# Kernel tuning notes

Hardware: AMD Instinct MI355X
Metric: run time of the kernel (lower is better)

Reference implementation:

```python
import jax, jax.numpy as jnp
import numpy as np

NEG = 10000.0

def setup_inputs() -> dict:
    key = jax.random.key(0)
    ks = jax.random.split(key, 5)
    B, S, D = 2, 2048, 1024
    std = 1.0 / np.sqrt(D)
    return {
        "x": jax.random.normal(ks[0], (B, S, D), dtype=jnp.float32),
        "Wq": jax.random.normal(ks[1], (D, D), dtype=jnp.float32) * std,
        "bq": jnp.zeros((D,), jnp.float32),
        "Wk": jax.random.normal(ks[2], (D, D), dtype=jnp.float32) * std,
        "bk": jnp.zeros((D,), jnp.float32),
        "Wv": jax.random.normal(ks[3], (D, D), dtype=jnp.float32) * std,
        "bv": jnp.zeros((D,), jnp.float32),
        "Wo": jax.random.normal(ks[4], (D, D), dtype=jnp.float32) * std,
        "bo": jnp.zeros((D,), jnp.float32),
    }

def reference(x, Wq, bq, Wk, bk, Wv, bv, Wo, bo):
    # Linear projections + relu activation (as in the keras layer; note: no head split
    # is performed in this implementation, head_num is only a divisibility check).
    q = jax.nn.relu(x @ Wq + bq)  # [B,S,D]
    k = jax.nn.relu(x @ Wk + bk)
    v = jax.nn.relu(x @ Wv + bv)
    D = q.shape[-1]
    e = jnp.einsum('bqd,bkd->bqk', q, k) / jnp.sqrt(jnp.float32(D))  # [B,S,S]
    # history_only causal mask: penalize key positions j > query position i
    S = e.shape[-1]
    causal = (jnp.arange(S)[None, :] > jnp.arange(S)[:, None]).astype(e.dtype)
    e = e - NEG * causal[None, :, :]
    # stable softmax exactly as in the source (max-subtract, exp, normalize)
    e = jnp.exp(e - jnp.max(e, axis=-1, keepdims=True))
    attn = e / jnp.sum(e, axis=-1, keepdims=True)
    y = jnp.einsum('bqk,bkd->bqd', attn, v)
    return jax.nn.relu(y @ Wo + bo)
```

## Files before the change

kernel.cpp:

```cpp
#include <hip/hip_runtime.h>
#include <math.h>


typedef _Float16 f16x8 __attribute__((ext_vector_type(8)));
typedef float f32x4 __attribute__((ext_vector_type(4)));

#define BK 32

__device__ __forceinline__ void gload_lds16(const void* g, void* l) {
  __builtin_amdgcn_global_load_lds(
      (const __attribute__((address_space(1))) void*)g,
      (__attribute__((address_space(3))) void*)l, 16, 0, 0);
}

template<bool RELU, bool HAS_BIAS, int CAUSAL, int TMp, int TNp, bool MULTI, typename OT>
__global__ __launch_bounds__(256) void gemm_f16(
    const _Float16* __restrict__ A, const _Float16* __restrict__ BT,
    const float* __restrict__ bias0, const float* __restrict__ bias1,
    const float* __restrict__ bias2,
    OT* __restrict__ C0, OT* __restrict__ C1, OT* __restrict__ C2,
    int M, int Nout, int K, float scale,
    long long sA, long long sB, long long sC)
{
  int m0, n0;
  if (CAUSAL == 1) {
    int bx = blockIdx.x;
    int i = (int)((sqrtf(4.f * bx + 1.f) - 1.f) * 0.5f);
    while ((i + 1) * (i + 2) <= bx) ++i;
    while (i * (i + 1) > bx) --i;
    int j = bx - i * (i + 1);
    m0 = i * TMp;
    n0 = j * TNp;
  } else {
    m0 = blockIdx.y * TMp;
    n0 = blockIdx.x * TNp;
  }
  A  += (long long)blockIdx.z * sA;
  BT += (long long)blockIdx.z * sB;
  const int kend = (CAUSAL == 2) ? ((m0 + TMp < K) ? m0 + TMp : K) : K;

  __shared__ _Float16 Ah[TMp * BK];
  __shared__ _Float16 Bh[TNp * BK];

  const int tid  = threadIdx.x;
  const int lane = tid & 63;
  const int wid  = tid >> 6;
  const int wm   = (wid >> 1) * (TMp / 2);
  const int wn   = (wid & 1) * (TNp / 2);
  const int l15  = lane & 15;
  const int quad = lane >> 4;
  constexpr int MT = TMp / 32;
  constexpr int NT = TNp / 32;

  f32x4 acc[MT][NT];
  #pragma unroll
  for (int i = 0; i < MT; ++i)
    #pragma unroll
    for (int j = 0; j < NT; ++j)
      acc[i][j] = (f32x4){0.f, 0.f, 0.f, 0.f};

  constexpr int AI = TMp / 64;
  constexpr int BI = TNp / 64;
  const int ar = wid * (TMp / 4);
  const int br = wid * (TNp / 4);
  const int rl = lane >> 2;
  const int kq = (lane & 3) * 8;

  for (int k0 = 0; k0 < kend; k0 += BK) {
    #pragma unroll
    for (int t = 0; t < AI; ++t)
      gload_lds16(A + (long long)(m0 + ar + t * 16 + rl) * K + k0 + kq,
                  Ah + (ar + t * 16) * BK);
    #pragma unroll
    for (int t = 0; t < BI; ++t)
      gload_lds16(BT + (long long)(n0 + br + t * 16 + rl) * K + k0 + kq,
                  Bh + (br + t * 16) * BK);
    __syncthreads();

    const f16x8* ap = (const f16x8*)(Ah + (wm + l15) * BK + quad * 8);
    const f16x8* bp = (const f16x8*)(Bh + (wn + l15) * BK + quad * 8);
    f16x8 af[MT], bf[NT];
    #pragma unroll
    for (int t = 0; t < MT; ++t) af[t] = ap[t * 64];
    #pragma unroll
    for (int t = 0; t < NT; ++t) bf[t] = bp[t * 64];
    #pragma unroll
    for (int mt = 0; mt < MT; ++mt)
      #pragma unroll
      for (int nt = 0; nt < NT; ++nt)
        acc[mt][nt] = __builtin_amdgcn_mfma_f32_16x16x32_f16(
            af[mt], bf[nt], acc[mt][nt], 0, 0, 0);
    __syncthreads();
  }

  const int mat = MULTI ? (n0 / Nout) : 0;
  const float* bias = HAS_BIAS ? (mat == 0 ? bias0 : (mat == 1 ? bias1 : bias2)) : nullptr;
  OT* C = (mat == 0 ? C0 : (mat == 1 ? C1 : C2)) + (long long)blockIdx.z * sC;
  const int c0 = MULTI ? (n0 - mat * Nout) : n0;

  float bvals[NT];
  if (HAS_BIAS) {
    #pragma unroll
    for (int nt = 0; nt < NT; ++nt)
      bvals[nt] = bias[c0 + wn + nt * 16 + l15];
  }
  #pragma unroll
  for (int mt = 0; mt < MT; ++mt) {
    #pragma unroll
    for (int nt = 0; nt < NT; ++nt) {
      const int col = c0 + wn + nt * 16 + l15;
      #pragma unroll
      for (int r = 0; r < 4; ++r) {
        const int row = m0 + wm + mt * 16 + quad * 4 + r;
        float v = acc[mt][nt][r] * scale;
        if (HAS_BIAS) v += bvals[nt];
        if (RELU) v = fmaxf(v, 0.f);
        C[(long long)row * Nout + col] = (OT)v;
      }
    }
  }
}

__global__ __launch_bounds__(256) void cvt_f32_f16(
    const float* __restrict__ in, _Float16* __restrict__ out)
{
  const long long i = ((long long)blockIdx.x * 256 + threadIdx.x) * 8;
  float4 a = *(const float4*)(in + i);
  float4 b = *(const float4*)(in + i + 4);
  f16x8 o = {(_Float16)a.x, (_Float16)a.y, (_Float16)a.z, (_Float16)a.w,
             (_Float16)b.x, (_Float16)b.y, (_Float16)b.z, (_Float16)b.w};
  *(f16x8*)(out + i) = o;
}

__global__ __launch_bounds__(256) void cvtT_all(
    const float* __restrict__ W0, const float* __restrict__ W1,
    const float* __restrict__ W2, const float* __restrict__ W3,
    _Float16* __restrict__ WT, int K, int N)
{
  __shared__ _Float16 t[64][72];
  const int z = blockIdx.z;
  const float* W = (z == 0) ? W0 : (z == 1) ? W1 : (z == 2) ? W2 : W3;
  _Float16* dst = WT + (long long)z * K * N;
  const int k0 = blockIdx.x * 64, n0 = blockIdx.y * 64;
  const int tid = threadIdx.x;
  #pragma unroll
  for (int it = 0; it < 4; ++it) {
    int idx = tid + it * 256;
    int r = idx >> 4, c4 = (idx & 15) << 2;
    float4 w = *(const float4*)(W + (long long)(k0 + r) * N + n0 + c4);
    t[r][c4 + 0] = (_Float16)w.x; t[r][c4 + 1] = (_Float16)w.y;
    t[r][c4 + 2] = (_Float16)w.z; t[r][c4 + 3] = (_Float16)w.w;
  }
  __syncthreads();
  #pragma unroll
  for (int it = 0; it < 2; ++it) {
    int idx = tid + it * 256;
    int r = idx >> 3, c8 = (idx & 7) << 3;
    f16x8 o;
    #pragma unroll
    for (int j = 0; j < 8; ++j) o[j] = t[c8 + j][r];
    *(f16x8*)(dst + (long long)(n0 + r) * K + k0 + c8) = o;
  }
}

__global__ __launch_bounds__(256) void transp_f16(
    const _Float16* __restrict__ V, _Float16* __restrict__ VT, int S, int D)
{
  __shared__ _Float16 t[64][72];
  const _Float16* Vb = V + (long long)blockIdx.z * S * D;
  _Float16* VTb = VT + (long long)blockIdx.z * D * S;
  const int s0 = blockIdx.x * 64, d0 = blockIdx.y * 64;
  const int tid = threadIdx.x;
  #pragma unroll
  for (int it = 0; it < 2; ++it) {
    int idx = tid + it * 256;
    int r = idx >> 3, c8 = (idx & 7) << 3;
    f16x8 v = *(const f16x8*)(Vb + (long long)(s0 + r) * D + d0 + c8);
    *(f16x8*)&t[r][c8] = v;
  }
  __syncthreads();
  #pragma unroll
  for (int it = 0; it < 2; ++it) {
    int idx = tid + it * 256;
    int r = idx >> 3, c8 = (idx & 7) << 3;
    f16x8 o;
    #pragma unroll
    for (int j = 0; j < 8; ++j) o[j] = t[c8 + j][r];
    *(f16x8*)(VTb + (long long)(d0 + r) * S + s0 + c8) = o;
  }
}

__global__ __launch_bounds__(256) void softmax_causal_h(
    _Float16* __restrict__ E, int S)
{
  const int i = blockIdx.x;
  _Float16* row = E + ((long long)blockIdx.y * S + i) * S;
  const int tid = threadIdx.x;
  const int n = i + 1;
  const int j0 = tid * 8;

  f16x8 hv = *(const f16x8*)(row + j0);
  float vals[8];
  float m = -3.0e38f;
  #pragma unroll
  for (int t = 0; t < 8; ++t) {
    float v = (j0 + t < n) ? (float)hv[t] : -3.0e38f;
    vals[t] = v;
    m = fmaxf(m, v);
  }
  #pragma unroll
  for (int o = 32; o > 0; o >>= 1) m = fmaxf(m, __shfl_down(m, o, 64));

  __shared__ float rmax[4];
  __shared__ float rsum[4];
  const int wave = tid >> 6;
  if ((tid & 63) == 0) rmax[wave] = m;
  __syncthreads();
  m = fmaxf(fmaxf(rmax[0], rmax[1]), fmaxf(rmax[2], rmax[3]));

  float s = 0.f;
  #pragma unroll
  for (int t = 0; t < 8; ++t) {
    float e = (j0 + t < n) ? expf(vals[t] - m) : 0.f;
    vals[t] = e;
    s += e;
  }
  #pragma unroll
  for (int o = 32; o > 0; o >>= 1) s += __shfl_down(s, o, 64);
  if ((tid & 63) == 0) rsum[wave] = s;
  __syncthreads();
  s = rsum[0] + rsum[1] + rsum[2] + rsum[3];

  const float inv = 1.0f / s;
  f16x8 ov;
  #pragma unroll
  for (int t = 0; t < 8; ++t) ov[t] = (_Float16)(vals[t] * inv);
  *(f16x8*)(row + j0) = ov;
}

extern "C" void kernel_launch(void* const* d_in, const int* in_sizes, int n_in,
                              void* d_out, int out_size, void* d_ws, size_t ws_size,
                              hipStream_t stream) {
  const float* x  = (const float*)d_in[0];
  const float* Wq = (const float*)d_in[1];
  const float* bq = (const float*)d_in[2];
  const float* Wk = (const float*)d_in[3];
  const float* bk = (const float*)d_in[4];
  const float* Wv = (const float*)d_in[5];
  const float* bv = (const float*)d_in[6];
  const float* Wo = (const float*)d_in[7];
  const float* bo = (const float*)d_in[8];
  float* out = (float*)d_out;

  const int Bn = 2, S = 2048, D = 1024;
  const int M = Bn * S;
  const size_t MD = (size_t)M * D;
  const size_t DD = (size_t)D * D;
  const size_t SS = (size_t)Bn * S * S;

  _Float16* ws   = (_Float16*)d_ws;
  _Float16* xh   = ws;
  _Float16* Wcat = xh + MD;
  _Float16* Qh   = Wcat + 4 * DD;
  _Float16* Kh   = Qh + MD;
  _Float16* Vh   = Kh + MD;
  _Float16* VTh  = Vh + MD;
  _Float16* E    = VTh + MD;
  _Float16* Yh   = E + SS;

  dim3 blk(256);

  cvt_f32_f16<<<dim3((unsigned)(MD / 2048)), blk, 0, stream>>>(x, xh);
  cvtT_all<<<dim3(D / 64, D / 64, 4), blk, 0, stream>>>(Wq, Wk, Wv, Wo, Wcat, D, D);

  gemm_f16<true, true, 0, 128, 128, true, _Float16>
      <<<dim3(3 * D / 128, M / 128), blk, 0, stream>>>(
      xh, Wcat, bq, bk, bv, Qh, Kh, Vh, M, D, D, 1.0f, 0, 0, 0);

  transp_f16<<<dim3(S / 64, D / 64, Bn), blk, 0, stream>>>(Vh, VTh, S, D);

  gemm_f16<false, false, 1, 128, 64, false, _Float16>
      <<<dim3(272, 1, Bn), blk, 0, stream>>>(
      Qh, Kh, nullptr, nullptr, nullptr, E, nullptr, nullptr,
      S, S, D, 0.03125f, (long long)S * D, (long long)S * D, (long long)S * S);

  softmax_causal_h<<<dim3(S, Bn), blk, 0, stream>>>(E, S);

  gemm_f16<false, false, 2, 64, 128, false, _Float16>
      <<<dim3(D / 128, S / 64, Bn), blk, 0, stream>>>(
      E, VTh, nullptr, nullptr, nullptr, Yh, nullptr, nullptr,
      S, D, S, 1.0f, (long long)S * S, (long long)D * S, (long long)S * D);

  gemm_f16<true, true, 0, 128, 64, false, float>
      <<<dim3(D / 64, M / 128), blk, 0, stream>>>(
      Yh, Wcat + 3 * DD, bo, nullptr, nullptr, out, nullptr, nullptr,
      M, D, D, 1.0f, 0, 0, 0);
}
```

Measured before the change: 235.1 us.

## Fold Wo into V via associativity, drop transpose, widen BK with swizzled LDS

Computes (V·Wo)^T per batch with a GEMM (Wo^T times V^T) and feeds it directly into the attention-times-V GEMM, which now applies bias and ReLU and writes the float output. This removes the separate V transpose kernel and the final output projection GEMM. It also doubles the K-tile to 64 and XOR-swizzles LDS chunks to avoid bank conflicts, trading more LDS per block for fewer barriers. The reassociation changes fp16 rounding order and the V·Wo product is stored in fp16.

```diff
diff --git a/kernel.cpp b/kernel.cpp
--- a/kernel.cpp
+++ b/kernel.cpp
@@ -5,7 +5,7 @@
 typedef _Float16 f16x8 __attribute__((ext_vector_type(8)));
 typedef float f32x4 __attribute__((ext_vector_type(4)));
 
-#define BK 32
+#define BK 64
 
 __device__ __forceinline__ void gload_lds16(const void* g, void* l) {
   __builtin_amdgcn_global_load_lds(
@@ -59,37 +59,42 @@
     for (int j = 0; j < NT; ++j)
       acc[i][j] = (f32x4){0.f, 0.f, 0.f, 0.f};
 
-  constexpr int AI = TMp / 64;
-  constexpr int BI = TNp / 64;
-  const int ar = wid * (TMp / 4);
-  const int br = wid * (TNp / 4);
-  const int rl = lane >> 2;
-  const int kq = (lane & 3) * 8;
+  constexpr int AI = TMp / 32;
+  constexpr int BI = TNp / 32;
+  const int rl8  = lane >> 3;
+  const int swk  = ((lane & 7) ^ rl8) * 8;
+  const int arow = wid * (TMp / 4);
+  const int brow = wid * (TNp / 4);
 
   for (int k0 = 0; k0 < kend; k0 += BK) {
     #pragma unroll
     for (int t = 0; t < AI; ++t)
-      gload_lds16(A + (long long)(m0 + ar + t * 16 + rl) * K + k0 + kq,
-                  Ah + (ar + t * 16) * BK);
+      gload_lds16(A + (long long)(m0 + arow + t * 8 + rl8) * K + k0 + swk,
+                  Ah + (arow + t * 8) * BK);
     #pragma unroll
     for (int t = 0; t < BI; ++t)
-      gload_lds16(BT + (long long)(n0 + br + t * 16 + rl) * K + k0 + kq,
-                  Bh + (br + t * 16) * BK);
+      gload_lds16(BT + (long long)(n0 + brow + t * 8 + rl8) * K + k0 + swk,
+                  Bh + (brow + t * 8) * BK);
     __syncthreads();
 
-    const f16x8* ap = (const f16x8*)(Ah + (wm + l15) * BK + quad * 8);
-    const f16x8* bp = (const f16x8*)(Bh + (wn + l15) * BK + quad * 8);
-    f16x8 af[MT], bf[NT];
-    #pragma unroll
-    for (int t = 0; t < MT; ++t) af[t] = ap[t * 64];
-    #pragma unroll
-    for (int t = 0; t < NT; ++t) bf[t] = bp[t * 64];
-    #pragma unroll
-    for (int mt = 0; mt < MT; ++mt)
-      #pragma unroll
-      for (int nt = 0; nt < NT; ++nt)
-        acc[mt][nt] = __builtin_amdgcn_mfma_f32_16x16x32_f16(
-            af[mt], bf[nt], acc[mt][nt], 0, 0, 0);
+    const _Float16* ab = Ah + (wm + l15) * BK;
+    const _Float16* bb = Bh + (wn + l15) * BK;
+    const int sw8 = l15 & 7;
+    #pragma unroll
+    for (int ko = 0; ko < 2; ++ko) {
+      const int ch = ((ko * 4 + quad) ^ sw8) * 8;
+      f16x8 af[MT], bf[NT];
+      #pragma unroll
+      for (int t = 0; t < MT; ++t) af[t] = *(const f16x8*)(ab + t * 16 * BK + ch);
+      #pragma unroll
+      for (int t = 0; t < NT; ++t) bf[t] = *(const f16x8*)(bb + t * 16 * BK + ch);
+      #pragma unroll
+      for (int mt = 0; mt < MT; ++mt)
+        #pragma unroll
+        for (int nt = 0; nt < NT; ++nt)
+          acc[mt][nt] = __builtin_amdgcn_mfma_f32_16x16x32_f16(
+              af[mt], bf[nt], acc[mt][nt], 0, 0, 0);
+    }
     __syncthreads();
   }
 
@@ -160,33 +165,6 @@
     #pragma unroll
     for (int j = 0; j < 8; ++j) o[j] = t[c8 + j][r];
     *(f16x8*)(dst + (long long)(n0 + r) * K + k0 + c8) = o;
-  }
-}
-
-__global__ __launch_bounds__(256) void transp_f16(
-    const _Float16* __restrict__ V, _Float16* __restrict__ VT, int S, int D)
-{
-  __shared__ _Float16 t[64][72];
-  const _Float16* Vb = V + (long long)blockIdx.z * S * D;
-  _Float16* VTb = VT + (long long)blockIdx.z * D * S;
-  const int s0 = blockIdx.x * 64, d0 = blockIdx.y * 64;
-  const int tid = threadIdx.x;
-  #pragma unroll
-  for (int it = 0; it < 2; ++it) {
-    int idx = tid + it * 256;
-    int r = idx >> 3, c8 = (idx & 7) << 3;
-    f16x8 v = *(const f16x8*)(Vb + (long long)(s0 + r) * D + d0 + c8);
-    *(f16x8*)&t[r][c8] = v;
-  }
-  __syncthreads();
-  #pragma unroll
-  for (int it = 0; it < 2; ++it) {
-    int idx = tid + it * 256;
-    int r = idx >> 3, c8 = (idx & 7) << 3;
-    f16x8 o;
-    #pragma unroll
-    for (int j = 0; j < 8; ++j) o[j] = t[c8 + j][r];
-    *(f16x8*)(VTb + (long long)(d0 + r) * S + s0 + c8) = o;
   }
 }
 
@@ -264,9 +242,8 @@
   _Float16* Qh   = Wcat + 4 * DD;
   _Float16* Kh   = Qh + MD;
   _Float16* Vh   = Kh + MD;
-  _Float16* VTh  = Vh + MD;
-  _Float16* E    = VTh + MD;
-  _Float16* Yh   = E + SS;
+  _Float16* VWT  = Vh + MD;
+  _Float16* E    = VWT + MD;
 
   dim3 blk(256);
 
@@ -276,23 +253,21 @@
   gemm_f16<true, true, 0, 128, 128, true, _Float16>
       <<<dim3(3 * D / 128, M / 128), blk, 0, stream>>>(
       xh, Wcat, bq, bk, bv, Qh, Kh, Vh, M, D, D, 1.0f, 0, 0, 0);
-
-  transp_f16<<<dim3(S / 64, D / 64, Bn), blk, 0, stream>>>(Vh, VTh, S, D);
 
   gemm_f16<false, false, 1, 128, 64, false, _Float16>
       <<<dim3(272, 1, Bn), blk, 0, stream>>>(
       Qh, Kh, nullptr, nullptr, nullptr, E, nullptr, nullptr,
       S, S, D, 0.03125f, (long long)S * D, (long long)S * D, (long long)S * S);
 
+  gemm_f16<false, false, 0, 128, 64, false, _Float16>
+      <<<dim3(S / 64, D / 128, Bn), blk, 0, stream>>>(
+      Wcat + 3 * DD, Vh, nullptr, nullptr, nullptr, VWT, nullptr, nullptr,
+      D, S, D, 1.0f, 0, (long long)S * D, (long long)D * S);
+
   softmax_causal_h<<<dim3(S, Bn), blk, 0, stream>>>(E, S);
 
-  gemm_f16<false, false, 2, 64, 128, false, _Float16>
+  gemm_f16<true, true, 2, 64, 128, false, float>
       <<<dim3(D / 128, S / 64, Bn), blk, 0, stream>>>(
-      E, VTh, nullptr, nullptr, nullptr, Yh, nullptr, nullptr,
+      E, VWT, bo, nullptr, nullptr, out, nullptr, nullptr,
       S, D, S, 1.0f, (long long)S * S, (long long)D * S, (long long)S * D);
-
-  gemm_f16<true, true, 0, 128, 64, false, float>
-      <<<dim3(D / 64, M / 128), blk, 0, stream>>>(
-      Yh, Wcat + 3 * DD, bo, nullptr, nullptr, out, nullptr, nullptr,
-      M, D, D, 1.0f, 0, 0, 0);
-}
+}
```

After: 209.3 us. -11.0%, faster.
